# Performance work log

Measured on AMD Instinct MI355X. Metric: run time of the kernel, lower is better.

## Reference

```python
import jax, jax.numpy as jnp
import numpy as np

N, IN_F, H, D = 3072, 512, 8, 64


def setup_inputs() -> dict:
    key = jax.random.key(0)
    k1, k2, k3, k4, k5 = jax.random.split(key, 5)
    x = jax.random.normal(k1, (N, IN_F), dtype=jnp.float32)
    adj = jax.random.randint(k2, (N, N), 0, 2, dtype=jnp.int32)
    # xavier-uniform-like scales
    s_W = (6.0 / (IN_F + H * D)) ** 0.5
    s_a = (6.0 / (H + D)) ** 0.5
    W = jax.random.uniform(k3, (H * D, IN_F), dtype=jnp.float32, minval=-s_W, maxval=s_W)
    a_src = jax.random.uniform(k4, (H, D), dtype=jnp.float32, minval=-s_a, maxval=s_a)
    a_dst = jax.random.uniform(k5, (H, D), dtype=jnp.float32, minval=-s_a, maxval=s_a)
    return {"x": x, "adj": adj, "W": W, "a_src": a_src, "a_dst": a_dst}


def reference(x, adj, W, a_src, a_dst):
    n = x.shape[0]
    Hh, d = a_src.shape
    h = (x @ W.T).reshape(n, Hh, d)                      # [n, H, d]
    e_src = jnp.einsum('nhd,hd->nh', h, a_src)           # [n, H]
    e_dst = jnp.einsum('nhd,hd->nh', h, a_dst)           # [n, H]
    e = e_src[:, None, :] + e_dst[None, :, :]            # [n, n, H], e[i,j]=src_i+dst_j
    e = jax.nn.leaky_relu(e, negative_slope=0.2)
    mask = (adj + jnp.eye(n, dtype=adj.dtype)) > 0       # [n, n]
    e = jnp.where(mask[:, :, None], e, -jnp.inf)
    alpha = jax.nn.softmax(e, axis=1)                    # softmax over j (neighbors)
    # out[i,h,d] = sum_j alpha[i,j,h] * h[j,h,d]  (dropout=0 / eval mode)
    out = jnp.einsum('ijh,jhd->ihd', alpha, h)
    return out.reshape(n, Hh * d)                        # concat=True
```

## Files before the change

### kernel.cpp

```cpp
#include <hip/hip_runtime.h>
#include <hip/hip_bf16.h>

typedef __bf16 bf16x8 __attribute__((ext_vector_type(8)));
typedef __bf16 bf16x4 __attribute__((ext_vector_type(4)));
typedef _Float16 half8 __attribute__((ext_vector_type(8)));
typedef _Float16 half4 __attribute__((ext_vector_type(4)));
typedef _Float16 half2v __attribute__((ext_vector_type(2)));
typedef float f32x4 __attribute__((ext_vector_type(4)));
typedef float f32x16 __attribute__((ext_vector_type(16)));

#define NROW 3072
#define NF 512
#define NH 8
#define ND 64
#define GEMM_BLOCKS 384

__device__ __forceinline__ unsigned gat_enc_key(float f) {
    unsigned u = __float_as_uint(f);
    return (f < 0.f) ? ~u : (u | 0x80000000u);
}
__device__ __forceinline__ float gat_dec_key(unsigned k) {
    unsigned u = (k & 0x80000000u) ? (k ^ 0x80000000u) : ~k;
    return __uint_as_float(u);
}

__global__ __launch_bounds__(256) void gat_prep(const float* __restrict__ x,
                                                const float* __restrict__ W,
                                                __bf16* __restrict__ xb,
                                                __bf16* __restrict__ Wb,
                                                unsigned* __restrict__ maxkey) {
    if (blockIdx.x == 0 && threadIdx.x < NH) maxkey[threadIdx.x] = 0u;
    int k = blockIdx.x * 256 + threadIdx.x;
    const float4* s; __bf16* d;
    if (k < 393216) { s = (const float4*)x; d = xb; }
    else { k -= 393216;  s = (const float4*)W; d = Wb; }
    float4 v = s[k];
    bf16x4 o = { (__bf16)v.x, (__bf16)v.y, (__bf16)v.z, (__bf16)v.w };
    *reinterpret_cast<bf16x4*>(d + k * 4) = o;
}

__global__ __launch_bounds__(256) void gat_gemm_bp(const __bf16* __restrict__ xb,
                                                   const __bf16* __restrict__ Wb,
                                                   _Float16* __restrict__ hT,
                                                   const int* __restrict__ adj,
                                                   unsigned long long* __restrict__ bits64) {
    __shared__ __align__(16) __bf16 sA[2][4096];
    __shared__ __align__(16) __bf16 sB[2][4096];

    if (blockIdx.x >= GEMM_BLOCKS) {
        int i = blockIdx.x - GEMM_BLOCKS;
        int wave = threadIdx.x >> 6;
        int lane = threadIdx.x & 63;
        const int* row = adj + i * NROW;
#pragma unroll
        for (int it = 0; it < 12; ++it) {
            int base = wave * 768 + it * 64;
            int j = base + lane;
            bool pred = (row[j] > 0) || (j == i);
            unsigned long long bal = __ballot(pred);
            if (lane == 0) bits64[i * 48 + (base >> 6)] = bal;
        }
        return;
    }

    int b = blockIdx.x;
    int i0 = (b >> 3) * 64;
    int o0 = (b & 7) * 64;
    int tid = threadIdx.x;
    int wave = tid >> 6;
    int lane = tid & 63;
    int half = lane >> 5;
    int l31 = lane & 31;
    int wr = wave >> 1;
    int wc = wave & 1;

    int v0 = tid, v1 = tid + 256;
    int r0 = v0 >> 3, r1 = v1 >> 3;
    int cc0 = ((v0 & 7) ^ (r0 & 7)) << 3;
    int cc1 = ((v1 & 7) ^ (r1 & 7)) << 3;
    const __bf16* gA0 = xb + (i0 + r0) * NF + cc0;
    const __bf16* gA1 = xb + (i0 + r1) * NF + cc1;
    const __bf16* gB0 = Wb + (o0 + r0) * NF + cc0;
    const __bf16* gB1 = Wb + (o0 + r1) * NF + cc1;

    {
        bf16x8 a0 = *reinterpret_cast<const bf16x8*>(gA0);
        bf16x8 a1 = *reinterpret_cast<const bf16x8*>(gA1);
        bf16x8 b0 = *reinterpret_cast<const bf16x8*>(gB0);
        bf16x8 b1 = *reinterpret_cast<const bf16x8*>(gB1);
        *reinterpret_cast<bf16x8*>(&sA[0][v0 * 8]) = a0;
        *reinterpret_cast<bf16x8*>(&sA[0][v1 * 8]) = a1;
        *reinterpret_cast<bf16x8*>(&sB[0][v0 * 8]) = b0;
        *reinterpret_cast<bf16x8*>(&sB[0][v1 * 8]) = b1;
    }
    __syncthreads();

    f32x16 acc = {};
    int arow = (wr * 32 + l31) * 64;
    int brow = (wc * 32 + l31) * 64;
    int sw7 = l31 & 7;

    for (int c = 0; c < 8; ++c) {
        bf16x8 na0, na1, nb0, nb1;
        bool more = (c < 7);
        if (more) {
            na0 = *reinterpret_cast<const bf16x8*>(gA0 + (c + 1) * 64);
            na1 = *reinterpret_cast<const bf16x8*>(gA1 + (c + 1) * 64);
            nb0 = *reinterpret_cast<const bf16x8*>(gB0 + (c + 1) * 64);
            nb1 = *reinterpret_cast<const bf16x8*>(gB1 + (c + 1) * 64);
        }
        const __bf16* pa = &sA[c & 1][0];
        const __bf16* pb = &sB[c & 1][0];
#pragma unroll
        for (int ks = 0; ks < 4; ++ks) {
            int q = (((ks << 1) | half) ^ sw7) << 3;
            bf16x8 a = *reinterpret_cast<const bf16x8*>(pa + arow + q);
            bf16x8 bb = *reinterpret_cast<const bf16x8*>(pb + brow + q);
            acc = __builtin_amdgcn_mfma_f32_32x32x16_bf16(a, bb, acc, 0, 0, 0);
        }
        if (more) {
            *reinterpret_cast<bf16x8*>(&sA[(c + 1) & 1][v0 * 8]) = na0;
            *reinterpret_cast<bf16x8*>(&sA[(c + 1) & 1][v1 * 8]) = na1;
            *reinterpret_cast<bf16x8*>(&sB[(c + 1) & 1][v0 * 8]) = nb0;
            *reinterpret_cast<bf16x8*>(&sB[(c + 1) & 1][v1 * 8]) = nb1;
        }
        __syncthreads();
    }

    _Float16* tt = reinterpret_cast<_Float16*>(&sA[0][0]) + wave * 1056;
#pragma unroll
    for (int reg = 0; reg < 16; ++reg) {
        int rowl = (reg & 3) + 8 * (reg >> 2) + 4 * half;
        tt[rowl * 33 + l31] = (_Float16)acc[reg];
    }
    __syncthreads();
    int orow = lane >> 1;
    int li = (lane & 1) * 16;
    half8 h0, h1;
#pragma unroll
    for (int t = 0; t < 8; ++t) h0[t] = tt[(li + t) * 33 + orow];
#pragma unroll
    for (int t = 0; t < 8; ++t) h1[t] = tt[(li + 8 + t) * 33 + orow];
    _Float16* op = hT + (long)(o0 + wc * 32 + orow) * NROW + i0 + wr * 32 + li;
    *reinterpret_cast<half8*>(op) = h0;
    *reinterpret_cast<half8*>(op + 8) = h1;
}

__global__ __launch_bounds__(256) void gat_edges(const _Float16* __restrict__ hT,
                                                 const float* __restrict__ a_src,
                                                 const float* __restrict__ a_dst,
                                                 float* __restrict__ e_srcT,
                                                 float* __restrict__ e_dstT,
                                                 unsigned* __restrict__ maxkey) {
    int hh = blockIdx.y;
    int i = blockIdx.x * 256 + threadIdx.x;
    float ps = 0.f, pd = 0.f;
#pragma unroll
    for (int d = 0; d < ND; ++d) {
        float hv = (float)hT[(hh * ND + d) * NROW + i];
        ps += hv * a_src[hh * ND + d];
        pd += hv * a_dst[hh * ND + d];
    }
    e_srcT[hh * NROW + i] = ps;
    e_dstT[hh * NROW + i] = pd;
    float mx = pd;
#pragma unroll
    for (int off = 1; off < 64; off <<= 1) mx = fmaxf(mx, __shfl_xor(mx, off, 64));
    if ((threadIdx.x & 63) == 0) atomicMax(&maxkey[hh], gat_enc_key(mx));
}

__global__ __launch_bounds__(256) void gat_attn(const unsigned* __restrict__ bits,
                                                const float* __restrict__ e_srcT,
                                                const float* __restrict__ e_dstT,
                                                const unsigned* __restrict__ maxkey,
                                                const _Float16* __restrict__ hT,
                                                _Float16* __restrict__ num,
                                                float* __restrict__ den) {
    constexpr int JCHUNK = NROW / 4;
    constexpr int NC = JCHUNK / 64;
    __shared__ unsigned lds_P[JCHUNK / 2];
    __shared__ unsigned lds_Q[JCHUNK / 2];
    __shared__ __align__(16) _Float16 hbuf[2][4096];
    int b = blockIdx.x;
    int head = b & 7;
    int jc = (b >> 3) & 3;
    int i0 = ((b >> 3) >> 2) * 128;
    int jbase = jc * JCHUNK;
    int tid = threadIdx.x;
    int wave = tid >> 6;
    int lane = tid & 63;
    int half = lane >> 5;
    int l31 = lane & 31;

    float Mg = gat_dec_key(maxkey[head]);
    for (int p = tid; p < JCHUNK / 2; p += 256) {
        float t0 = e_dstT[head * NROW + jbase + 2 * p] - Mg;
        float t1 = e_dstT[head * NROW + jbase + 2 * p + 1] - Mg;
        half2v P = { (_Float16)__expf(t0), (_Float16)__expf(t1) };
        half2v Q = { (_Float16)__expf(0.2f * t0), (_Float16)__expf(0.2f * t1) };
        lds_P[p] = __builtin_bit_cast(unsigned, P);
        lds_Q[p] = __builtin_bit_cast(unsigned, Q);
    }

    int irow = i0 + wave * 32 + l31;
    float u = e_srcT[head * NROW + irow] + Mg;
    float Af = (u > 0.f) ? 1.f : __expf(0.8f * u);
    float Cf = (u > 0.f) ? __expf(-0.8f * u) : 1.f;
    _Float16 Ah = (_Float16)Af, Ch = (_Float16)Cf;
    half2v A2 = { Ah, Ah };
    half2v C2 = { Ch, Ch };
    const half8 ones8 = { (_Float16)1.f, (_Float16)1.f, (_Float16)1.f, (_Float16)1.f,
                          (_Float16)1.f, (_Float16)1.f, (_Float16)1.f, (_Float16)1.f };
    const unsigned* brow = bits + irow * 96 + jc * (JCHUNK / 32);

    int s0 = tid, s1 = tid + 256;
    const _Float16* gp0 = hT + (head * ND + ((s0 >> 6) & 1) * 32 + (s0 & 31)) * NROW
                             + jbase + (s0 >> 7) * 16 + ((s0 >> 5) & 1) * 8;
    const _Float16* gp1 = hT + (head * ND + ((s1 >> 6) & 1) * 32 + (s1 & 31)) * NROW
                             + jbase + (s1 >> 7) * 16 + ((s1 >> 5) & 1) * 8;
    *reinterpret_cast<half8*>(&hbuf[0][tid * 8])         = *reinterpret_cast<const half8*>(gp0);
    *reinterpret_cast<half8*>(&hbuf[0][(tid + 256) * 8]) = *reinterpret_cast<const half8*>(gp1);
    __syncthreads();

    f32x16 acc0 = {};
    f32x16 acc1 = {};
    f32x16 acc2 = {};
    uint2 wm = *reinterpret_cast<const uint2*>(brow);

    for (int k = 0; k < NC; ++k) {
        half8 st0, st1;
        uint2 wmn = wm;
        bool more = (k + 1 < NC);
        if (more) {
            st0 = *reinterpret_cast<const half8*>(gp0 + (k + 1) * 64);
            st1 = *reinterpret_cast<const half8*>(gp1 + (k + 1) * 64);
            wmn = *reinterpret_cast<const uint2*>(brow + (k + 1) * 2);
        }
        const _Float16* hb = &hbuf[k & 1][0];
#pragma unroll
        for (int js = 0; js < 4; ++js) {
            unsigned word = (js < 2) ? wm.x : wm.y;
            unsigned w8 = (word >> ((js & 1) * 16 + half * 8)) & 0xffu;
            uint4 Pv = *reinterpret_cast<const uint4*>(&lds_P[k * 32 + js * 8 + half * 4]);
            uint4 Qv = *reinterpret_cast<const uint4*>(&lds_Q[k * 32 + js * 8 + half * 4]);
            unsigned pr[4] = { Pv.x, Pv.y, Pv.z, Pv.w };
            unsigned qr[4] = { Qv.x, Qv.y, Qv.z, Qv.w };
            unsigned am[4];
#pragma unroll
            for (int t = 0; t < 4; ++t) {
                half2v pp = __builtin_bit_cast(half2v, pr[t]) * A2;
                half2v qq = __builtin_bit_cast(half2v, qr[t]) * C2;
                half2v mx = __builtin_elementwise_max(pp, qq);
                int b0 = ((int)(w8 << (31 - 2 * t))) >> 31;
                int b1 = ((int)(w8 << (30 - 2 * t))) >> 31;
                unsigned mk = ((unsigned)b0 & 0xFFFFu) | ((unsigned)b1 & 0xFFFF0000u);
                am[t] = __builtin_bit_cast(unsigned, mx) & mk;
            }
            uint4 m4 = { am[0], am[1], am[2], am[3] };
            half8 af = __builtin_bit_cast(half8, m4);
            half8 v0 = *reinterpret_cast<const half8*>(hb + (js * 128 + lane) * 8);
            half8 v1 = *reinterpret_cast<const half8*>(hb + (js * 128 + 64 + lane) * 8);
            acc0 = __builtin_amdgcn_mfma_f32_32x32x16_f16(af, v0, acc0, 0, 0, 0);
            acc1 = __builtin_amdgcn_mfma_f32_32x32x16_f16(af, v1, acc1, 0, 0, 0);
            acc2 = __builtin_amdgcn_mfma_f32_32x32x16_f16(af, ones8, acc2, 0, 0, 0);
        }
        if (more) {
            *reinterpret_cast<half8*>(&hbuf[(k + 1) & 1][tid * 8])         = st0;
            *reinterpret_cast<half8*>(&hbuf[(k + 1) & 1][(tid + 256) * 8]) = st1;
        }
        wm = wmn;
        __syncthreads();
    }

    if (l31 == 0) {
#pragma unroll
        for (int reg = 0; reg < 16; ++reg) {
            int rowl = (reg & 3) + 8 * (reg >> 2) + 4 * half;
            den[(long)(jc * NROW + i0 + wave * 32 + rowl) * NH + head] = acc2[reg];
        }
    }

#pragma unroll
    for (int reg = 0; reg < 16; ++reg) {
        int rowl = (reg & 3) + 8 * (reg >> 2) + 4 * half;
        long ob = (long)(jc * NROW + i0 + wave * 32 + rowl) * NF + head * ND + l31;
        num[ob]      = (_Float16)acc0[reg];
        num[ob + 32] = (_Float16)acc1[reg];
    }
}

__global__ __launch_bounds__(256) void gat_final(const _Float16* __restrict__ num,
                                                 const float* __restrict__ den,
                                                 float* __restrict__ out) {
    int idx = (blockIdx.x * 256 + threadIdx.x) * 8;
    int i = idx >> 9;
    int c = idx & 511;
    int head = c >> 6;
    half8 n0 = *reinterpret_cast<const half8*>(num + (long)i * NF + c);
    half8 n1 = *reinterpret_cast<const half8*>(num + (long)(NROW + i) * NF + c);
    half8 n2 = *reinterpret_cast<const half8*>(num + (long)(2 * NROW + i) * NF + c);
    half8 n3 = *reinterpret_cast<const half8*>(num + (long)(3 * NROW + i) * NF + c);
    float ds = den[i * NH + head] + den[(NROW + i) * NH + head]
             + den[(2 * NROW + i) * NH + head] + den[(3 * NROW + i) * NH + head];
    float inv = 1.0f / fmaxf(ds, 1e-30f);
    float r0 = ((float)n0[0] + (float)n1[0] + (float)n2[0] + (float)n3[0]) * inv;
    float r1 = ((float)n0[1] + (float)n1[1] + (float)n2[1] + (float)n3[1]) * inv;
    float r2 = ((float)n0[2] + (float)n1[2] + (float)n2[2] + (float)n3[2]) * inv;
    float r3 = ((float)n0[3] + (float)n1[3] + (float)n2[3] + (float)n3[3]) * inv;
    float r4 = ((float)n0[4] + (float)n1[4] + (float)n2[4] + (float)n3[4]) * inv;
    float r5 = ((float)n0[5] + (float)n1[5] + (float)n2[5] + (float)n3[5]) * inv;
    float r6 = ((float)n0[6] + (float)n1[6] + (float)n2[6] + (float)n3[6]) * inv;
    float r7 = ((float)n0[7] + (float)n1[7] + (float)n2[7] + (float)n3[7]) * inv;
    float4 o0 = { r0, r1, r2, r3 };
    float4 o1 = { r4, r5, r6, r7 };
    *reinterpret_cast<float4*>(out + idx)     = o0;
    *reinterpret_cast<float4*>(out + idx + 4) = o1;
}

extern "C" void kernel_launch(void* const* d_in, const int* in_sizes, int n_in,
                              void* d_out, int out_size, void* d_ws, size_t ws_size,
                              hipStream_t stream) {
    const float* x_raw  = (const float*)d_in[0];
    const int*   adj    = (const int*)d_in[1];
    const float* W_raw  = (const float*)d_in[2];
    const float* as_raw = (const float*)d_in[3];
    const float* ad_raw = (const float*)d_in[4];
    float* out = (float*)d_out;

    char* ws = (char*)d_ws;
    _Float16* hT     = (_Float16*)(ws);
    float*    e_srcT = (float*)(ws + 3145728);
    float*    e_dstT = (float*)(ws + 3244032);
    unsigned* maxkey = (unsigned*)(ws + 3342336);
    unsigned* bits   = (unsigned*)(ws + 3342400);
    __bf16*   xb     = (__bf16*)(ws + 4522048);
    __bf16*   Wb     = (__bf16*)(ws + 7667776);
    _Float16* num    = (_Float16*)(ws + 8192064);
    float*    den    = (float*)(ws + 20774976);

    gat_prep<<<1792, 256, 0, stream>>>(x_raw, W_raw, xb, Wb, maxkey);
    gat_gemm_bp<<<GEMM_BLOCKS + NROW, 256, 0, stream>>>(xb, Wb, hT, adj,
                                                        (unsigned long long*)bits);
    gat_edges<<<dim3(12, 8), 256, 0, stream>>>(hT, as_raw, ad_raw, e_srcT, e_dstT, maxkey);
    gat_attn<<<24 * 4 * 8, 256, 0, stream>>>(bits, e_srcT, e_dstT, maxkey, hT, num, den);
    gat_final<<<NROW * NF / 2048, 256, 0, stream>>>(num, den, out);
}
```

Before: 140.7 us.

## Fuse fp32-to-bf16 conversion and edge-score reduction into projection GEMM kernel

Drops the separate bf16 conversion kernel: the GEMM now loads fp32 x and W directly and converts them while staging into shared memory. The per-node e_src/e_dst dot products and the per-head max are computed in the GEMM epilogue from the transposed tile, which removes the gat_edges kernel and its re-read of hT. In the attention kernel the two-factor leaky-relu exponent scaling becomes a single clamped ratio multiply, and mask extraction is simplified. The fused GEMM loads twice as many bytes per tile from global memory, and the clamp on the ratio adds fp16 range risk.

```diff
diff --git a/kernel.cpp b/kernel.cpp
--- a/kernel.cpp
+++ b/kernel.cpp
@@ -2,10 +2,9 @@
 #include <hip/hip_bf16.h>
 
 typedef __bf16 bf16x8 __attribute__((ext_vector_type(8)));
-typedef __bf16 bf16x4 __attribute__((ext_vector_type(4)));
 typedef _Float16 half8 __attribute__((ext_vector_type(8)));
-typedef _Float16 half4 __attribute__((ext_vector_type(4)));
 typedef _Float16 half2v __attribute__((ext_vector_type(2)));
+typedef short s16x2 __attribute__((ext_vector_type(2)));
 typedef float f32x4 __attribute__((ext_vector_type(4)));
 typedef float f32x16 __attribute__((ext_vector_type(16)));
 
@@ -24,28 +23,27 @@
     return __uint_as_float(u);
 }
 
-__global__ __launch_bounds__(256) void gat_prep(const float* __restrict__ x,
-                                                const float* __restrict__ W,
-                                                __bf16* __restrict__ xb,
-                                                __bf16* __restrict__ Wb,
-                                                unsigned* __restrict__ maxkey) {
-    if (blockIdx.x == 0 && threadIdx.x < NH) maxkey[threadIdx.x] = 0u;
-    int k = blockIdx.x * 256 + threadIdx.x;
-    const float4* s; __bf16* d;
-    if (k < 393216) { s = (const float4*)x; d = xb; }
-    else { k -= 393216;  s = (const float4*)W; d = Wb; }
-    float4 v = s[k];
-    bf16x4 o = { (__bf16)v.x, (__bf16)v.y, (__bf16)v.z, (__bf16)v.w };
-    *reinterpret_cast<bf16x4*>(d + k * 4) = o;
-}
-
-__global__ __launch_bounds__(256) void gat_gemm_bp(const __bf16* __restrict__ xb,
-                                                   const __bf16* __restrict__ Wb,
+__device__ __forceinline__ bf16x8 gat_ld_cvt8(const float* p) {
+    float4 f0 = *reinterpret_cast<const float4*>(p);
+    float4 f1 = *reinterpret_cast<const float4*>(p + 4);
+    bf16x8 o = { (__bf16)f0.x, (__bf16)f0.y, (__bf16)f0.z, (__bf16)f0.w,
+                 (__bf16)f1.x, (__bf16)f1.y, (__bf16)f1.z, (__bf16)f1.w };
+    return o;
+}
+
+__global__ __launch_bounds__(256) void gat_gemm_bp(const float* __restrict__ x,
+                                                   const float* __restrict__ W,
                                                    _Float16* __restrict__ hT,
                                                    const int* __restrict__ adj,
-                                                   unsigned long long* __restrict__ bits64) {
+                                                   unsigned long long* __restrict__ bits64,
+                                                   const float* __restrict__ a_src,
+                                                   const float* __restrict__ a_dst,
+                                                   float* __restrict__ e_srcT,
+                                                   float* __restrict__ e_dstT,
+                                                   unsigned* __restrict__ maxkey) {
     __shared__ __align__(16) __bf16 sA[2][4096];
     __shared__ __align__(16) __bf16 sB[2][4096];
+    __shared__ float ered[2][2][2][32];
 
     if (blockIdx.x >= GEMM_BLOCKS) {
         int i = blockIdx.x - GEMM_BLOCKS;
@@ -66,6 +64,7 @@
     int b = blockIdx.x;
     int i0 = (b >> 3) * 64;
     int o0 = (b & 7) * 64;
+    int head = b & 7;
     int tid = threadIdx.x;
     int wave = tid >> 6;
     int lane = tid & 63;
@@ -78,21 +77,15 @@
     int r0 = v0 >> 3, r1 = v1 >> 3;
     int cc0 = ((v0 & 7) ^ (r0 & 7)) << 3;
     int cc1 = ((v1 & 7) ^ (r1 & 7)) << 3;
-    const __bf16* gA0 = xb + (i0 + r0) * NF + cc0;
-    const __bf16* gA1 = xb + (i0 + r1) * NF + cc1;
-    const __bf16* gB0 = Wb + (o0 + r0) * NF + cc0;
-    const __bf16* gB1 = Wb + (o0 + r1) * NF + cc1;
-
-    {
-        bf16x8 a0 = *reinterpret_cast<const bf16x8*>(gA0);
-        bf16x8 a1 = *reinterpret_cast<const bf16x8*>(gA1);
-        bf16x8 b0 = *reinterpret_cast<const bf16x8*>(gB0);
-        bf16x8 b1 = *reinterpret_cast<const bf16x8*>(gB1);
-        *reinterpret_cast<bf16x8*>(&sA[0][v0 * 8]) = a0;
-        *reinterpret_cast<bf16x8*>(&sA[0][v1 * 8]) = a1;
-        *reinterpret_cast<bf16x8*>(&sB[0][v0 * 8]) = b0;
-        *reinterpret_cast<bf16x8*>(&sB[0][v1 * 8]) = b1;
-    }
+    const float* gA0 = x + (i0 + r0) * NF + cc0;
+    const float* gA1 = x + (i0 + r1) * NF + cc1;
+    const float* gB0 = W + (o0 + r0) * NF + cc0;
+    const float* gB1 = W + (o0 + r1) * NF + cc1;
+
+    *reinterpret_cast<bf16x8*>(&sA[0][v0 * 8]) = gat_ld_cvt8(gA0);
+    *reinterpret_cast<bf16x8*>(&sA[0][v1 * 8]) = gat_ld_cvt8(gA1);
+    *reinterpret_cast<bf16x8*>(&sB[0][v0 * 8]) = gat_ld_cvt8(gB0);
+    *reinterpret_cast<bf16x8*>(&sB[0][v1 * 8]) = gat_ld_cvt8(gB1);
     __syncthreads();
 
     f32x16 acc = {};
@@ -104,10 +97,10 @@
         bf16x8 na0, na1, nb0, nb1;
         bool more = (c < 7);
         if (more) {
-            na0 = *reinterpret_cast<const bf16x8*>(gA0 + (c + 1) * 64);
-            na1 = *reinterpret_cast<const bf16x8*>(gA1 + (c + 1) * 64);
-            nb0 = *reinterpret_cast<const bf16x8*>(gB0 + (c + 1) * 64);
-            nb1 = *reinterpret_cast<const bf16x8*>(gB1 + (c + 1) * 64);
+            na0 = gat_ld_cvt8(gA0 + (c + 1) * 64);
+            na1 = gat_ld_cvt8(gA1 + (c + 1) * 64);
+            nb0 = gat_ld_cvt8(gB0 + (c + 1) * 64);
+            nb1 = gat_ld_cvt8(gB1 + (c + 1) * 64);
         }
         const __bf16* pa = &sA[c & 1][0];
         const __bf16* pb = &sB[c & 1][0];
@@ -127,46 +120,60 @@
         __syncthreads();
     }
 
-    _Float16* tt = reinterpret_cast<_Float16*>(&sA[0][0]) + wave * 1056;
+    _Float16* tt = reinterpret_cast<_Float16*>(&sA[0][0]) + wave * 1280;
 #pragma unroll
     for (int reg = 0; reg < 16; ++reg) {
         int rowl = (reg & 3) + 8 * (reg >> 2) + 4 * half;
-        tt[rowl * 33 + l31] = (_Float16)acc[reg];
-    }
-    __syncthreads();
+        tt[rowl * 40 + l31] = (_Float16)acc[reg];
+    }
     int orow = lane >> 1;
     int li = (lane & 1) * 16;
     half8 h0, h1;
 #pragma unroll
-    for (int t = 0; t < 8; ++t) h0[t] = tt[(li + t) * 33 + orow];
-#pragma unroll
-    for (int t = 0; t < 8; ++t) h1[t] = tt[(li + 8 + t) * 33 + orow];
+    for (int t = 0; t < 8; ++t) h0[t] = tt[(li + t) * 40 + orow];
+#pragma unroll
+    for (int t = 0; t < 8; ++t) h1[t] = tt[(li + 8 + t) * 40 + orow];
     _Float16* op = hT + (long)(o0 + wc * 32 + orow) * NROW + i0 + wr * 32 + li;
     *reinterpret_cast<half8*>(op) = h0;
     *reinterpret_cast<half8*>(op + 8) = h1;
-}
-
-__global__ __launch_bounds__(256) void gat_edges(const _Float16* __restrict__ hT,
-                                                 const float* __restrict__ a_src,
-                                                 const float* __restrict__ a_dst,
-                                                 float* __restrict__ e_srcT,
-                                                 float* __restrict__ e_dstT,
-                                                 unsigned* __restrict__ maxkey) {
-    int hh = blockIdx.y;
-    int i = blockIdx.x * 256 + threadIdx.x;
+
+    half8 hv0 = *reinterpret_cast<const half8*>(tt + l31 * 40 + half * 16);
+    half8 hv1 = *reinterpret_cast<const half8*>(tt + l31 * 40 + half * 16 + 8);
+    const float* ap = a_src + head * ND + wc * 32 + half * 16;
+    const float* dp = a_dst + head * ND + wc * 32 + half * 16;
+    float4 as0 = *reinterpret_cast<const float4*>(ap);
+    float4 as1 = *reinterpret_cast<const float4*>(ap + 4);
+    float4 as2 = *reinterpret_cast<const float4*>(ap + 8);
+    float4 as3 = *reinterpret_cast<const float4*>(ap + 12);
+    float4 ad0 = *reinterpret_cast<const float4*>(dp);
+    float4 ad1 = *reinterpret_cast<const float4*>(dp + 4);
+    float4 ad2 = *reinterpret_cast<const float4*>(dp + 8);
+    float4 ad3 = *reinterpret_cast<const float4*>(dp + 12);
     float ps = 0.f, pd = 0.f;
-#pragma unroll
-    for (int d = 0; d < ND; ++d) {
-        float hv = (float)hT[(hh * ND + d) * NROW + i];
-        ps += hv * a_src[hh * ND + d];
-        pd += hv * a_dst[hh * ND + d];
-    }
-    e_srcT[hh * NROW + i] = ps;
-    e_dstT[hh * NROW + i] = pd;
-    float mx = pd;
-#pragma unroll
-    for (int off = 1; off < 64; off <<= 1) mx = fmaxf(mx, __shfl_xor(mx, off, 64));
-    if ((threadIdx.x & 63) == 0) atomicMax(&maxkey[hh], gat_enc_key(mx));
+    ps += (float)hv0[0]*as0.x + (float)hv0[1]*as0.y + (float)hv0[2]*as0.z + (float)hv0[3]*as0.w;
+    ps += (float)hv0[4]*as1.x + (float)hv0[5]*as1.y + (float)hv0[6]*as1.z + (float)hv0[7]*as1.w;
+    ps += (float)hv1[0]*as2.x + (float)hv1[1]*as2.y + (float)hv1[2]*as2.z + (float)hv1[3]*as2.w;
+    ps += (float)hv1[4]*as3.x + (float)hv1[5]*as3.y + (float)hv1[6]*as3.z + (float)hv1[7]*as3.w;
+    pd += (float)hv0[0]*ad0.x + (float)hv0[1]*ad0.y + (float)hv0[2]*ad0.z + (float)hv0[3]*ad0.w;
+    pd += (float)hv0[4]*ad1.x + (float)hv0[5]*ad1.y + (float)hv0[6]*ad1.z + (float)hv0[7]*ad1.w;
+    pd += (float)hv1[0]*ad2.x + (float)hv1[1]*ad2.y + (float)hv1[2]*ad2.z + (float)hv1[3]*ad2.w;
+    pd += (float)hv1[4]*ad3.x + (float)hv1[5]*ad3.y + (float)hv1[6]*ad3.z + (float)hv1[7]*ad3.w;
+    ps += __shfl_xor(ps, 32, 64);
+    pd += __shfl_xor(pd, 32, 64);
+    if (half == 0) { ered[0][wr][wc][l31] = ps; ered[1][wr][wc][l31] = pd; }
+    __syncthreads();
+    if (wc == 0) {
+        float pst = ered[0][wr][0][l31] + ered[0][wr][1][l31];
+        float pdt = ered[1][wr][0][l31] + ered[1][wr][1][l31];
+        if (half == 0) {
+            e_srcT[head * NROW + i0 + wr * 32 + l31] = pst;
+            e_dstT[head * NROW + i0 + wr * 32 + l31] = pdt;
+        }
+        float mx = pdt;
+#pragma unroll
+        for (int off = 1; off < 32; off <<= 1) mx = fmaxf(mx, __shfl_xor(mx, off, 64));
+        if (lane == 0) atomicMax(&maxkey[head], gat_enc_key(mx));
+    }
 }
 
 __global__ __launch_bounds__(256) void gat_attn(const unsigned* __restrict__ bits,
@@ -204,11 +211,9 @@
 
     int irow = i0 + wave * 32 + l31;
     float u = e_srcT[head * NROW + irow] + Mg;
-    float Af = (u > 0.f) ? 1.f : __expf(0.8f * u);
-    float Cf = (u > 0.f) ? __expf(-0.8f * u) : 1.f;
-    _Float16 Ah = (_Float16)Af, Ch = (_Float16)Cf;
-    half2v A2 = { Ah, Ah };
-    half2v C2 = { Ch, Ch };
+    float Rf = fminf(__expf(-0.8f * u), 60000.f);
+    _Float16 Rh = (_Float16)Rf;
+    half2v R2 = { Rh, Rh };
     const half8 ones8 = { (_Float16)1.f, (_Float16)1.f, (_Float16)1.f, (_Float16)1.f,
                           (_Float16)1.f, (_Float16)1.f, (_Float16)1.f, (_Float16)1.f };
     const unsigned* brow = bits + irow * 96 + jc * (JCHUNK / 32);
@@ -241,6 +246,8 @@
         for (int js = 0; js < 4; ++js) {
             unsigned word = (js < 2) ? wm.x : wm.y;
             unsigned w8 = (word >> ((js & 1) * 16 + half * 8)) & 0xffu;
+            unsigned long long S64 = ((unsigned long long)(w8 & 0x55u) << 15)
+                                   | ((unsigned long long)(w8 & 0xAAu) << 30);
             uint4 Pv = *reinterpret_cast<const uint4*>(&lds_P[k * 32 + js * 8 + half * 4]);
             uint4 Qv = *reinterpret_cast<const uint4*>(&lds_Q[k * 32 + js * 8 + half * 4]);
             unsigned pr[4] = { Pv.x, Pv.y, Pv.z, Pv.w };
@@ -248,13 +255,13 @@
             unsigned am[4];
 #pragma unroll
             for (int t = 0; t < 4; ++t) {
-                half2v pp = __builtin_bit_cast(half2v, pr[t]) * A2;
-                half2v qq = __builtin_bit_cast(half2v, qr[t]) * C2;
-                half2v mx = __builtin_elementwise_max(pp, qq);
-                int b0 = ((int)(w8 << (31 - 2 * t))) >> 31;
-                int b1 = ((int)(w8 << (30 - 2 * t))) >> 31;
-                unsigned mk = ((unsigned)b0 & 0xFFFFu) | ((unsigned)b1 & 0xFFFF0000u);
-                am[t] = __builtin_bit_cast(unsigned, mx) & mk;
+                half2v qq = __builtin_bit_cast(half2v, qr[t]) * R2;
+                half2v mx = __builtin_elementwise_max(
+                                __builtin_bit_cast(half2v, pr[t]), qq);
+                unsigned Wt = (unsigned)(S64 >> (2 * t));
+                s16x2 mks = __builtin_bit_cast(s16x2, Wt) >> 15;
+                am[t] = __builtin_bit_cast(unsigned, mx)
+                      & __builtin_bit_cast(unsigned, mks);
             }
             uint4 m4 = { am[0], am[1], am[2], am[3] };
             half8 af = __builtin_bit_cast(half8, m4);
@@ -272,17 +279,11 @@
         __syncthreads();
     }
 
-    if (l31 == 0) {
-#pragma unroll
-        for (int reg = 0; reg < 16; ++reg) {
-            int rowl = (reg & 3) + 8 * (reg >> 2) + 4 * half;
-            den[(long)(jc * NROW + i0 + wave * 32 + rowl) * NH + head] = acc2[reg];
-        }
-    }
-
 #pragma unroll
     for (int reg = 0; reg < 16; ++reg) {
         int rowl = (reg & 3) + 8 * (reg >> 2) + 4 * half;
+        if (l31 == 0)
+            den[(long)(jc * NROW + i0 + wave * 32 + rowl) * NH + head] = acc2[reg];
         long ob = (long)(jc * NROW + i0 + wave * 32 + rowl) * NF + head * ND + l31;
         num[ob]      = (_Float16)acc0[reg];
         num[ob + 32] = (_Float16)acc1[reg];
@@ -333,15 +334,14 @@
     float*    e_dstT = (float*)(ws + 3244032);
     unsigned* maxkey = (unsigned*)(ws + 3342336);
     unsigned* bits   = (unsigned*)(ws + 3342400);
-    __bf16*   xb     = (__bf16*)(ws + 4522048);
-    __bf16*   Wb     = (__bf16*)(ws + 7667776);
     _Float16* num    = (_Float16*)(ws + 8192064);
     float*    den    = (float*)(ws + 20774976);
 
-    gat_prep<<<1792, 256, 0, stream>>>(x_raw, W_raw, xb, Wb, maxkey);
-    gat_gemm_bp<<<GEMM_BLOCKS + NROW, 256, 0, stream>>>(xb, Wb, hT, adj,
-                                                        (unsigned long long*)bits);
-    gat_edges<<<dim3(12, 8), 256, 0, stream>>>(hT, as_raw, ad_raw, e_srcT, e_dstT, maxkey);
+    hipMemsetAsync(maxkey, 0, 64, stream);
+    gat_gemm_bp<<<GEMM_BLOCKS + NROW, 256, 0, stream>>>(x_raw, W_raw, hT, adj,
+                                                        (unsigned long long*)bits,
+                                                        as_raw, ad_raw,
+                                                        e_srcT, e_dstT, maxkey);
     gat_attn<<<24 * 4 * 8, 256, 0, stream>>>(bits, e_srcT, e_dstT, maxkey, hT, num, den);
     gat_final<<<NROW * NF / 2048, 256, 0, stream>>>(num, den, out);
 }
```

Result: no change. 143.3 us (+1.9%).
